# Kernel tuning notes

Hardware: AMD Instinct MI355X
Metric: run time of the kernel (lower is better)

Reference implementation:

```python
import jax, jax.numpy as jnp
import numpy as np

EPS = 1e-5

def layer_norm(x, gamma, beta):
    mu = jnp.mean(x, axis=-1, keepdims=True)
    var = jnp.mean(jnp.square(x - mu), axis=-1, keepdims=True)
    return (x - mu) * jax.lax.rsqrt(var + EPS) * gamma + beta

def setup_inputs() -> dict:
    key = jax.random.key(0)
    ks = jax.random.split(key, 10)
    B, I, H = 4096, 2048, 2048
    G = 4 * H
    s_ih = 1.0 / np.sqrt(I)
    s_hh = 1.0 / np.sqrt(H)
    b_ih = jax.random.uniform(ks[4], (G,), jnp.float32, -s_ih, s_ih)
    b_hh = jax.random.uniform(ks[5], (G,), jnp.float32, -s_hh, s_hh)
    # forget-gate bias init to 1.0 (slot [H:2H] per the torch code's chunk order)
    b_ih = b_ih.at[H:2*H].set(1.0)
    b_hh = b_hh.at[H:2*H].set(1.0)
    return {
        "x": jax.random.normal(ks[0], (B, I), jnp.float32),
        "h_prev": jax.random.normal(ks[1], (B, H), jnp.float32),
        "c_prev": jax.random.normal(ks[2], (B, H), jnp.float32),
        "W_ih": jax.random.normal(ks[3], (I, G), jnp.float32) * s_ih,
        "W_hh": jax.random.normal(ks[6], (H, G), jnp.float32) * s_hh,
        "b_ih": b_ih,
        "b_hh": b_hh,
        "g_x": jnp.ones((G,), jnp.float32),
        "beta_x": jnp.zeros((G,), jnp.float32),
        "g_c": jnp.ones((H,), jnp.float32),
        "beta_c": jnp.zeros((H,), jnp.float32),
        "g_h": jnp.ones((H,), jnp.float32),
        "beta_h": jnp.zeros((H,), jnp.float32),
    }

def reference(x, h_prev, c_prev, W_ih, W_hh, b_ih, b_hh, g_x, beta_x, g_c, beta_c, g_h, beta_h):
    gates_x = layer_norm(x @ W_ih + b_ih, g_x, beta_x)   # LN only on input-path gates
    gates = gates_x + (h_prev @ W_hh + b_hh)              # [B, 4H]
    i_g, f_g, gg, o_g = jnp.split(gates, 4, axis=1)
    i_t = jax.nn.sigmoid(i_g)
    f_t = jax.nn.sigmoid(f_g)
    g_t = jnp.tanh(gg)
    o_t = jax.nn.sigmoid(o_g)
    c_t = layer_norm(f_t * c_prev + i_t * g_t, g_c, beta_c)
    h_t = layer_norm(o_t * jnp.tanh(c_t), g_h, beta_h)
    return (h_t, c_t)
```

## Files before the change

kernel.cpp:

```cpp
#include <hip/hip_runtime.h>
#include <stdint.h>

typedef unsigned short ushort_t;
typedef __attribute__((ext_vector_type(8))) short short8;
typedef __attribute__((ext_vector_type(4))) float f32x4;
typedef __attribute__((ext_vector_type(4))) ushort_t u16x4;

#define M_ROWS 4096
#define K_DIM  2048
#define N_GATE 8192
#define H_DIM  2048

__device__ __forceinline__ ushort_t f2bf(float f) {
    uint32_t u = __float_as_uint(f);
    uint32_t r = (u + 0x7FFFu + ((u >> 16) & 1u)) >> 16;
    return (ushort_t)r;
}
__device__ __forceinline__ float bf2f(ushort_t b) {
    return __uint_as_float(((uint32_t)b) << 16);
}
__device__ __forceinline__ float sigf(float x) {
    return 1.0f / (1.0f + __expf(-x));
}
__device__ __forceinline__ float tanh_fast(float x) {
    float e = __expf(2.0f * x);
    return 1.0f - 2.0f / (e + 1.0f);
}

__global__ void cvt_f32_bf16(const float* __restrict__ in, ushort_t* __restrict__ out, int n) {
    int i = (blockIdx.x * blockDim.x + threadIdx.x) * 4;
    if (i >= n) return;
    float4 v = *(const float4*)(in + i);
    u16x4 o;
    o[0] = f2bf(v.x); o[1] = f2bf(v.y); o[2] = f2bf(v.z); o[3] = f2bf(v.w);
    *(u16x4*)(out + i) = o;
}

__global__ void transpose_cvt(const float* __restrict__ W, ushort_t* __restrict__ Wt,
                              int K, int N) {
    __shared__ float tile[32][33];
    int bn = blockIdx.x * 32;
    int bk = blockIdx.y * 32;
    int tx = threadIdx.x;
    int ty = threadIdx.y;
#pragma unroll
    for (int i = 0; i < 32; i += 8)
        tile[ty + i][tx] = W[(size_t)(bk + ty + i) * N + bn + tx];
    __syncthreads();
#pragma unroll
    for (int i = 0; i < 32; i += 8)
        Wt[(size_t)(bn + ty + i) * K + bk + tx] = f2bf(tile[tx][ty + i]);
}

#define TBK 64

__global__ __launch_bounds__(512, 2) void gemm256_8ph(
    const ushort_t* __restrict__ A0, const ushort_t* __restrict__ B0, ushort_t* __restrict__ C0,
    const ushort_t* __restrict__ A1, const ushort_t* __restrict__ B1, ushort_t* __restrict__ C1,
    int M, int N, int K) {
    extern __shared__ char smem[];
    const ushort_t* A  = blockIdx.z ? A1 : A0;
    const ushort_t* Bt = blockIdx.z ? B1 : B0;
    ushort_t*       C  = blockIdx.z ? C1 : C0;

    const int t    = threadIdx.x;
    const int lane = t & 63, wid = t >> 6;
    const int wm   = wid >> 2, wn = wid & 3;
    const int l15  = lane & 15;
    const int l4c  = (lane >> 4) * 16;

    const int brow = blockIdx.y * 256;
    const int bcol = blockIdx.x * 256;

    const int srow = t >> 3;
    const int scol = (((t & 7) ^ ((t >> 3) & 7)) * 8);
    const ushort_t* gA = A  + (size_t)(brow + srow) * K + scol;
    const ushort_t* gB = Bt + (size_t)(bcol + srow) * K + scol;
    const int ldsw = wid * 1024;

    int aR[4], abit[4], bR[2], bbit[2];
#pragma unroll
    for (int fm = 0; fm < 4; ++fm) { int r = wm * 64 + fm * 16 + l15; aR[fm] = r * 128; abit[fm] = (r & 7) << 4; }
#pragma unroll
    for (int fn = 0; fn < 2; ++fn) { int r = wn * 32 + fn * 16 + l15; bR[fn] = r * 128; bbit[fn] = (r & 7) << 4; }

    f32x4 acc[8][4];
#pragma unroll
    for (int i = 0; i < 8; ++i)
#pragma unroll
        for (int j = 0; j < 4; ++j) acc[i][j] = f32x4{0.f, 0.f, 0.f, 0.f};

    short8 a[4][2], b0[2][2], b1[2][2];

#define STAGE_A(tt, h, buf) { _Pragma("unroll") for (int j = 0; j < 2; ++j) \
    __builtin_amdgcn_global_load_lds( \
        (const __attribute__((address_space(1))) void*)(gA + ((size_t)((h) * 128 + j * 64)) * K + (size_t)(tt) * TBK), \
        (__attribute__((address_space(3))) void*)(smem + (buf) * 65536 + (h) * 16384 + j * 8192 + ldsw), 16, 0, 0); }
#define STAGE_B(tt, h, buf) { _Pragma("unroll") for (int j = 0; j < 2; ++j) \
    __builtin_amdgcn_global_load_lds( \
        (const __attribute__((address_space(1))) void*)(gB + ((size_t)((h) * 128 + j * 64)) * K + (size_t)(tt) * TBK), \
        (__attribute__((address_space(3))) void*)(smem + 32768 + (buf) * 65536 + (h) * 16384 + j * 8192 + ldsw), 16, 0, 0); }
#define LDA(mh, buf) { _Pragma("unroll") for (int fm = 0; fm < 4; ++fm) _Pragma("unroll") for (int ks = 0; ks < 2; ++ks) \
    a[fm][ks] = *(const short8*)(smem + (buf) * 65536 + (mh) * 16384 + aR[fm] + ((ks * 64 + l4c) ^ abit[fm])); }
#define LDB(dst, nh, buf) { _Pragma("unroll") for (int fn = 0; fn < 2; ++fn) _Pragma("unroll") for (int ks = 0; ks < 2; ++ks) \
    dst[fn][ks] = *(const short8*)(smem + 32768 + (buf) * 65536 + (nh) * 16384 + bR[fn] + ((ks * 64 + l4c) ^ bbit[fn])); }
#define BARRIER() __builtin_amdgcn_s_barrier()
#define LGKM0()  { asm volatile("s_waitcnt lgkmcnt(0)" ::: "memory"); __builtin_amdgcn_sched_barrier(0); }
#define VM6()    asm volatile("s_waitcnt vmcnt(6)" ::: "memory")
#define MM(mh, nh, bb) { __builtin_amdgcn_s_setprio(1); \
    _Pragma("unroll") for (int ks = 0; ks < 2; ++ks) \
    _Pragma("unroll") for (int fm = 0; fm < 4; ++fm) \
    _Pragma("unroll") for (int fn = 0; fn < 2; ++fn) \
        acc[(mh) * 4 + fm][(nh) * 2 + fn] = __builtin_amdgcn_mfma_f32_16x16x32_bf16( \
            a[fm][ks], bb[fn][ks], acc[(mh) * 4 + fm][(nh) * 2 + fn], 0, 0, 0); \
    __builtin_amdgcn_s_setprio(0); }

    STAGE_A(0, 0, 0); STAGE_B(0, 0, 0); STAGE_B(0, 1, 0); STAGE_A(0, 1, 0);
    STAGE_A(1, 0, 1); STAGE_B(1, 0, 1); STAGE_B(1, 1, 1);
    VM6();
    BARRIER();

    const int NT = K / TBK;
    for (int tt = 0; tt < NT; tt += 2) {
        const int s2 = (tt + 2) & (NT - 1);
        const int s3 = (tt + 3) & (NT - 1);
        LDA(0, 0); LDB(b0, 0, 0);
        STAGE_A(tt + 1, 1, 1);
        BARRIER(); LGKM0(); MM(0, 0, b0); BARRIER();
        LDB(b1, 1, 0);
        STAGE_A(s2, 0, 0);
        BARRIER(); LGKM0(); MM(0, 1, b1); BARRIER();
        LDA(1, 0);
        STAGE_B(s2, 0, 0);
        BARRIER(); LGKM0(); MM(1, 0, b0); BARRIER();
        STAGE_B(s2, 1, 0);
        VM6();
        BARRIER(); LGKM0(); MM(1, 1, b1); BARRIER();
        LDA(0, 1); LDB(b0, 0, 1);
        STAGE_A(s2, 1, 0);
        BARRIER(); LGKM0(); MM(0, 0, b0); BARRIER();
        LDB(b1, 1, 1);
        STAGE_A(s3, 0, 1);
        BARRIER(); LGKM0(); MM(0, 1, b1); BARRIER();
        LDA(1, 1);
        STAGE_B(s3, 0, 1);
        BARRIER(); LGKM0(); MM(1, 0, b0); BARRIER();
        STAGE_B(s3, 1, 1);
        VM6();
        BARRIER(); LGKM0(); MM(1, 1, b1); BARRIER();
    }

#pragma unroll
    for (int i = 0; i < 8; ++i) {
        const int mh = i >> 2, fm = i & 3;
        const int row0 = brow + mh * 128 + wm * 64 + fm * 16 + (lane >> 4) * 4;
#pragma unroll
        for (int jn = 0; jn < 4; ++jn) {
            const int nh = jn >> 1, fn = jn & 1;
            const int col = bcol + nh * 128 + wn * 32 + fn * 16 + l15;
#pragma unroll
            for (int r = 0; r < 4; ++r)
                C[(size_t)(row0 + r) * N + col] = f2bf(acc[i][jn][r]);
        }
    }
#undef STAGE_A
#undef STAGE_B
#undef LDA
#undef LDB
#undef BARRIER
#undef LGKM0
#undef VM6
#undef MM
}

__device__ __forceinline__ void block_reduce2(float& a, float& b, float* sred, int t) {
#pragma unroll
    for (int o = 32; o; o >>= 1) {
        a += __shfl_down(a, o);
        b += __shfl_down(b, o);
    }
    __syncthreads();
    if ((t & 63) == 0) { int w = t >> 6; sred[w] = a; sred[4 + w] = b; }
    __syncthreads();
    a = sred[0] + sred[1] + sred[2] + sred[3];
    b = sred[4] + sred[5] + sred[6] + sred[7];
}

__global__ __launch_bounds__(256) void fuse_ln_lstm(
    const ushort_t* __restrict__ xW, const ushort_t* __restrict__ hW,
    const float* __restrict__ c_prev,
    const float* __restrict__ b_ih, const float* __restrict__ b_hh,
    const float* __restrict__ g_x, const float* __restrict__ beta_x,
    const float* __restrict__ g_c, const float* __restrict__ beta_c,
    const float* __restrict__ g_h, const float* __restrict__ beta_h,
    float* __restrict__ h_out, float* __restrict__ c_out) {

    __shared__ float sgx[N_GATE];
    __shared__ float scell[H_DIM];
    __shared__ float sot[H_DIM];
    __shared__ float sred[8];

    const int b = blockIdx.x;
    const int t = threadIdx.x;
    const ushort_t* xwr = xW + (size_t)b * N_GATE;
    const ushort_t* hwr = hW + (size_t)b * N_GATE;
    const float*    cpr = c_prev + (size_t)b * H_DIM;

    float s = 0.f, q = 0.f;
#pragma unroll
    for (int it = 0; it < 4; ++it) {
        int idx = it * 2048 + t * 8;
        short8 v = *(const short8*)&xwr[idx];
#pragma unroll
        for (int j = 0; j < 8; ++j) {
            float f = bf2f((ushort_t)v[j]) + b_ih[idx + j];
            sgx[idx + j] = f;
            s += f; q += f * f;
        }
    }
    block_reduce2(s, q, sred, t);
    const float inv_g = 1.0f / (float)N_GATE;
    float mu   = s * inv_g;
    float rstd = rsqrtf(q * inv_g - mu * mu + 1e-5f);

    float cs = 0.f, cq = 0.f;
#pragma unroll
    for (int it = 0; it < 8; ++it) {
        int j = it * 256 + t;
        int ji = j, jf = j + 2048, jg = j + 4096, jo = j + 6144;
        float gi = (sgx[ji] - mu) * rstd * g_x[ji] + beta_x[ji] + bf2f(hwr[ji]) + b_hh[ji];
        float gf = (sgx[jf] - mu) * rstd * g_x[jf] + beta_x[jf] + bf2f(hwr[jf]) + b_hh[jf];
        float gg = (sgx[jg] - mu) * rstd * g_x[jg] + beta_x[jg] + bf2f(hwr[jg]) + b_hh[jg];
        float go = (sgx[jo] - mu) * rstd * g_x[jo] + beta_x[jo] + bf2f(hwr[jo]) + b_hh[jo];
        float i_t = sigf(gi);
        float f_t = sigf(gf);
        float g_t = tanh_fast(gg);
        float o_t = sigf(go);
        float cell = f_t * cpr[j] + i_t * g_t;
        scell[j] = cell;
        sot[j]   = o_t;
        cs += cell; cq += cell * cell;
    }
    block_reduce2(cs, cq, sred, t);
    const float inv_h = 1.0f / (float)H_DIM;
    float muc   = cs * inv_h;
    float rstdc = rsqrtf(cq * inv_h - muc * muc + 1e-5f);

    float hs = 0.f, hq = 0.f;
#pragma unroll
    for (int it = 0; it < 8; ++it) {
        int j = it * 256 + t;
        float ct = (scell[j] - muc) * rstdc * g_c[j] + beta_c[j];
        c_out[(size_t)b * H_DIM + j] = ct;
        float hp = sot[j] * tanh_fast(ct);
        sgx[j] = hp;
        hs += hp; hq += hp * hp;
    }
    block_reduce2(hs, hq, sred, t);
    float muh   = hs * inv_h;
    float rstdh = rsqrtf(hq * inv_h - muh * muh + 1e-5f);

#pragma unroll
    for (int it = 0; it < 8; ++it) {
        int j = it * 256 + t;
        h_out[(size_t)b * H_DIM + j] = (sgx[j] - muh) * rstdh * g_h[j] + beta_h[j];
    }
}

extern "C" void kernel_launch(void* const* d_in, const int* in_sizes, int n_in,
                              void* d_out, int out_size, void* d_ws, size_t ws_size,
                              hipStream_t stream) {
    const float* x      = (const float*)d_in[0];
    const float* h_prev = (const float*)d_in[1];
    const float* c_prev = (const float*)d_in[2];
    const float* W_ih   = (const float*)d_in[3];
    const float* W_hh   = (const float*)d_in[4];
    const float* b_ih   = (const float*)d_in[5];
    const float* b_hh   = (const float*)d_in[6];
    const float* g_x    = (const float*)d_in[7];
    const float* beta_x = (const float*)d_in[8];
    const float* g_c    = (const float*)d_in[9];
    const float* beta_c = (const float*)d_in[10];
    const float* g_h    = (const float*)d_in[11];
    const float* beta_h = (const float*)d_in[12];

    const int M = M_ROWS, K = K_DIM, N = N_GATE;

    ushort_t* Xb   = (ushort_t*)d_ws;
    ushort_t* Hb   = Xb   + (size_t)M * K;
    ushort_t* WihT = Hb   + (size_t)M * K;
    ushort_t* WhhT = WihT + (size_t)N * K;
    ushort_t* xWb  = WhhT + (size_t)N * K;
    ushort_t* hWb  = xWb  + (size_t)M * N;

    const int n_xh = M * K;
    cvt_f32_bf16<<<n_xh / (256 * 4), 256, 0, stream>>>(x,      Xb, n_xh);
    cvt_f32_bf16<<<n_xh / (256 * 4), 256, 0, stream>>>(h_prev, Hb, n_xh);

    transpose_cvt<<<dim3(N / 32, K / 32), dim3(32, 8), 0, stream>>>(W_ih, WihT, K, N);
    transpose_cvt<<<dim3(N / 32, K / 32), dim3(32, 8), 0, stream>>>(W_hh, WhhT, K, N);

    static int lds_attr_set = 0;
    if (!lds_attr_set) {
        (void)hipFuncSetAttribute(reinterpret_cast<const void*>(&gemm256_8ph),
                                  hipFuncAttributeMaxDynamicSharedMemorySize, 131072);
        lds_attr_set = 1;
    }
    gemm256_8ph<<<dim3(N / 256, M / 256, 2), 512, 131072, stream>>>(
        Xb, WihT, xWb, Hb, WhhT, hWb, M, N, K);

    float* h_out = (float*)d_out;
    float* c_out = h_out + (size_t)M * H_DIM;
    fuse_ln_lstm<<<M, 256, 0, stream>>>(xWb, hWb, c_prev, b_ih, b_hh,
                                        g_x, beta_x, g_c, beta_c, g_h, beta_h,
                                        h_out, c_out);
}
```

Measured before the change: 364.6 us.

## Stage GEMM epilogue through LDS, swizzle block order, merge prep launches

The GEMM epilogue now writes bf16 results into swizzled LDS and then stores full 16-byte rows to global memory, replacing scattered 2-byte stores. Workgroup indices are remapped so that consecutive blocks are spread across XCD-like groups, which is meant to improve L2 locality. The two conversion kernels and the two transpose kernels are each merged into a single launch using an extra grid dimension. In exchange the epilogue adds an LDS round trip and two barriers, and the remap hardcodes 32 column tiles.

```diff
diff --git a/kernel.cpp b/kernel.cpp
--- a/kernel.cpp
+++ b/kernel.cpp
@@ -27,7 +27,10 @@
     return 1.0f - 2.0f / (e + 1.0f);
 }
 
-__global__ void cvt_f32_bf16(const float* __restrict__ in, ushort_t* __restrict__ out, int n) {
+__global__ void cvt2_f32_bf16(const float* __restrict__ in0, ushort_t* __restrict__ out0,
+                              const float* __restrict__ in1, ushort_t* __restrict__ out1, int n) {
+    const float* in  = blockIdx.y ? in1 : in0;
+    ushort_t*    out = blockIdx.y ? out1 : out0;
     int i = (blockIdx.x * blockDim.x + threadIdx.x) * 4;
     if (i >= n) return;
     float4 v = *(const float4*)(in + i);
@@ -36,8 +39,11 @@
     *(u16x4*)(out + i) = o;
 }
 
-__global__ void transpose_cvt(const float* __restrict__ W, ushort_t* __restrict__ Wt,
-                              int K, int N) {
+__global__ void transpose_cvt2(const float* __restrict__ W0, ushort_t* __restrict__ Wt0,
+                               const float* __restrict__ W1, ushort_t* __restrict__ Wt1,
+                               int K, int N) {
+    const float* W  = blockIdx.z ? W1 : W0;
+    ushort_t*    Wt = blockIdx.z ? Wt1 : Wt0;
     __shared__ float tile[32][33];
     int bn = blockIdx.x * 32;
     int bk = blockIdx.y * 32;
@@ -69,8 +75,10 @@
     const int l15  = lane & 15;
     const int l4c  = (lane >> 4) * 16;
 
-    const int brow = blockIdx.y * 256;
-    const int bcol = blockIdx.x * 256;
+    const int linear = blockIdx.y * gridDim.x + blockIdx.x;
+    const int swz    = (linear & 7) * (int)((gridDim.x * gridDim.y) >> 3) + (linear >> 3);
+    const int brow = (swz >> 5) * 256;
+    const int bcol = (swz & 31) * 256;
 
     const int srow = t >> 3;
     const int scol = (((t & 7) ^ ((t >> 3) & 7)) * 8);
@@ -150,18 +158,32 @@
         BARRIER(); LGKM0(); MM(1, 1, b1); BARRIER();
     }
 
+    asm volatile("s_waitcnt vmcnt(0)" ::: "memory");
+    BARRIER();
 #pragma unroll
     for (int i = 0; i < 8; ++i) {
         const int mh = i >> 2, fm = i & 3;
-        const int row0 = brow + mh * 128 + wm * 64 + fm * 16 + (lane >> 4) * 4;
+        const int rbase = mh * 128 + wm * 64 + fm * 16 + (lane >> 4) * 4;
 #pragma unroll
         for (int jn = 0; jn < 4; ++jn) {
             const int nh = jn >> 1, fn = jn & 1;
-            const int col = bcol + nh * 128 + wn * 32 + fn * 16 + l15;
-#pragma unroll
-            for (int r = 0; r < 4; ++r)
-                C[(size_t)(row0 + r) * N + col] = f2bf(acc[i][jn][r]);
+            const int colb = (nh * 128 + wn * 32 + fn * 16 + l15) * 2;
+#pragma unroll
+            for (int r = 0; r < 4; ++r) {
+                const int row = rbase + r;
+                *(ushort_t*)(smem + row * 512 + (colb ^ ((row & 7) << 4))) = f2bf(acc[i][jn][r]);
+            }
         }
+    }
+    BARRIER();
+    {
+        const int row   = t >> 1;
+        const int halfb = (t & 1) * 256;
+        ushort_t* gout = C + (size_t)(brow + row) * N + bcol + (t & 1) * 128;
+#pragma unroll
+        for (int c = 0; c < 16; ++c)
+            *(short8*)(gout + c * 8) =
+                *(const short8*)(smem + row * 512 + ((halfb + c * 16) ^ ((row & 7) << 4)));
     }
 #undef STAGE_A
 #undef STAGE_B
@@ -294,11 +316,10 @@
     ushort_t* hWb  = xWb  + (size_t)M * N;
 
     const int n_xh = M * K;
-    cvt_f32_bf16<<<n_xh / (256 * 4), 256, 0, stream>>>(x,      Xb, n_xh);
-    cvt_f32_bf16<<<n_xh / (256 * 4), 256, 0, stream>>>(h_prev, Hb, n_xh);
-
-    transpose_cvt<<<dim3(N / 32, K / 32), dim3(32, 8), 0, stream>>>(W_ih, WihT, K, N);
-    transpose_cvt<<<dim3(N / 32, K / 32), dim3(32, 8), 0, stream>>>(W_hh, WhhT, K, N);
+    cvt2_f32_bf16<<<dim3(n_xh / (256 * 4), 2), 256, 0, stream>>>(x, Xb, h_prev, Hb, n_xh);
+
+    transpose_cvt2<<<dim3(N / 32, K / 32, 2), dim3(32, 8), 0, stream>>>(
+        W_ih, WihT, W_hh, WhhT, K, N);
 
     static int lds_attr_set = 0;
     if (!lds_attr_set) {
```

Result: slower. 393.0 us (+7.8%).
